# Optimization experiments

Measured on AMD Instinct MI355X. Metric: run time of the kernel, lower is better.

Reference implementation:

```python
import jax, jax.numpy as jnp
import numpy as np

B, C, U, N = 8, 64, 3, 512


def setup_inputs() -> dict:
    key = jax.random.key(0)
    k1, k2, k3, k4 = jax.random.split(key, 4)
    x = jax.random.normal(k1, (B, C, U, N), dtype=jnp.float32)
    # nn.Linear weights [out, in], applied as x @ W.T over channel dim
    s = 1.0 / np.sqrt(C)
    Wq = jax.random.uniform(k2, (C, C), dtype=jnp.float32, minval=-s, maxval=s)
    Wk = jax.random.uniform(k3, (C, C), dtype=jnp.float32, minval=-s, maxval=s)
    Wv = jax.random.uniform(k4, (C, C), dtype=jnp.float32, minval=-s, maxval=s)
    return {"x": x, "Wq": Wq, "Wk": Wk, "Wv": Wv}


def reference(x, Wq, Wk, Wv):
    # VNLinear: Linear over channel dim (dim 1), no bias: out[b,d,u,n] = sum_c x[b,c,u,n] W[d,c]
    def vn_linear(t, W):
        return jnp.einsum('bcun,dc->bdun', t, W)

    q = vn_linear(x, Wq)
    k = vn_linear(x, Wk)
    v = vn_linear(x, Wv)
    scale = x.shape[1] ** (-0.5)  # in_channels^-0.5
    # contraction over tiny vector-neuron dim u=3
    attn_logits = jnp.einsum('bcui,bcuj->bcij', q, k) * scale  # [B,C,N,N]
    attn_weights = jax.nn.softmax(attn_logits, axis=-1)
    out = jnp.einsum('bcij,bcuj->bcui', attn_weights, v)  # [B,C,U,N]
    return x + out
```

## Files before the change

### kernel.cpp

```cpp
#include <hip/hip_runtime.h>

#define BB 8
#define CC 64
#define UU 3
#define NN 512
#define POS (UU * NN)
#define QKV_ELEMS (BB * CC * POS)
#define SCALE2 0.1803368801111793f

__global__ __launch_bounds__(256) void proj_kernel(
    const float* __restrict__ x,
    const float* __restrict__ Wq,
    const float* __restrict__ Wk,
    const float* __restrict__ Wv,
    float* __restrict__ ws)
{
    const int blk   = blockIdx.x;
    const int bd2   = blk / 6;
    const int chunk = blk % 6;
    const int b     = bd2 >> 5;
    const int d0    = (bd2 & 31) * 2;
    const int tid   = threadIdx.x;
    const int p     = chunk * 256 + tid;

    __shared__ float w[6][CC];
    if (tid < 128) {
        int r = tid >> 6, c = tid & 63;
        w[r][c]     = Wq[(d0 + r) * CC + c];
        w[2 + r][c] = Wk[(d0 + r) * CC + c];
        w[4 + r][c] = Wv[(d0 + r) * CC + c];
    }
    __syncthreads();

    const float* xb = x + (size_t)b * CC * POS + p;
    float q0 = 0.f, q1 = 0.f, k0 = 0.f, k1 = 0.f, v0 = 0.f, v1 = 0.f;
    #pragma unroll 8
    for (int c = 0; c < CC; ++c) {
        float xv = xb[c * POS];
        q0 = fmaf(xv, w[0][c], q0);
        q1 = fmaf(xv, w[1][c], q1);
        k0 = fmaf(xv, w[2][c], k0);
        k1 = fmaf(xv, w[3][c], k1);
        v0 = fmaf(xv, w[4][c], v0);
        v1 = fmaf(xv, w[5][c], v1);
    }

    float* qs = ws;
    float* ks = ws + QKV_ELEMS;
    float* vs = ws + 2 * QKV_ELEMS;
    size_t base = (size_t)(b * CC + d0) * POS + p;
    qs[base] = q0 * SCALE2;  qs[base + POS] = q1 * SCALE2;
    ks[base] = k0;           ks[base + POS] = k1;
    vs[base] = v0;           vs[base + POS] = v1;
}

__global__ __launch_bounds__(256) void attn_kernel(
    const float* __restrict__ x,
    const float* __restrict__ ws,
    float* __restrict__ out)
{
    const int blk  = blockIdx.x;
    const int bd   = blk >> 1;
    const int half = blk & 1;
    const int tid  = threadIdx.x;

    __shared__ __align__(16) float ks[UU][NN];
    __shared__ __align__(16) float vs[UU][NN];
    __shared__ float4 part[NN / 2];

    const float* qsg = ws + (size_t)bd * POS;
    const float* ksg = ws + QKV_ELEMS     + (size_t)bd * POS;
    const float* vsg = ws + 2 * QKV_ELEMS + (size_t)bd * POS;

    {
        const float4* kg4 = (const float4*)ksg;
        const float4* vg4 = (const float4*)vsg;
        float4* ks4 = (float4*)&ks[0][0];
        float4* vs4 = (float4*)&vs[0][0];
        #pragma unroll
        for (int it = 0; it < 3; ++it) {
            int idx = tid + it * 256;
            if (idx < 384) ks4[idx] = kg4[idx];
            else           vs4[idx - 384] = vg4[idx - 384];
        }
    }
    __syncthreads();

    const int h    = tid & 3;
    const int slot = tid >> 2;

    float q0[4], q1[4], q2[4];
    #pragma unroll
    for (int m = 0; m < 4; ++m) {
        int i = half * 256 + slot + m * 64;
        q0[m] = qsg[i];
        q1[m] = qsg[NN + i];
        q2[m] = qsg[2 * NN + i];
    }

    float l[4]  = {0.f, 0.f, 0.f, 0.f};
    float a0[4] = {0.f, 0.f, 0.f, 0.f};
    float a1[4] = {0.f, 0.f, 0.f, 0.f};
    float a2[4] = {0.f, 0.f, 0.f, 0.f};

    const float4* k0p = (const float4*)&ks[0][0] + h * 32;
    const float4* k1p = (const float4*)&ks[1][0] + h * 32;
    const float4* k2p = (const float4*)&ks[2][0] + h * 32;
    const float4* v0p = (const float4*)&vs[0][0] + h * 32;
    const float4* v1p = (const float4*)&vs[1][0] + h * 32;
    const float4* v2p = (const float4*)&vs[2][0] + h * 32;
    const int t0 = 2 * h;

    #pragma unroll 2
    for (int tt = 0; tt < 32; ++tt) {
        const int t = (tt + t0) & 31;
        float4 k0 = k0p[t];
        float4 k1 = k1p[t];
        float4 k2 = k2p[t];
        float4 v0 = v0p[t];
        float4 v1 = v1p[t];
        float4 v2 = v2p[t];

        #pragma unroll
        for (int m = 0; m < 4; ++m) {
            float s0 = fmaf(q0[m], k0.x, fmaf(q1[m], k1.x, q2[m] * k2.x));
            float s1 = fmaf(q0[m], k0.y, fmaf(q1[m], k1.y, q2[m] * k2.y));
            float s2 = fmaf(q0[m], k0.z, fmaf(q1[m], k1.z, q2[m] * k2.z));
            float s3 = fmaf(q0[m], k0.w, fmaf(q1[m], k1.w, q2[m] * k2.w));

            float p0 = __builtin_amdgcn_exp2f(s0);
            float p1 = __builtin_amdgcn_exp2f(s1);
            float p2 = __builtin_amdgcn_exp2f(s2);
            float p3 = __builtin_amdgcn_exp2f(s3);

            l[m] += (p0 + p1) + (p2 + p3);
            a0[m] = fmaf(p0, v0.x, fmaf(p1, v0.y, fmaf(p2, v0.z, fmaf(p3, v0.w, a0[m]))));
            a1[m] = fmaf(p0, v1.x, fmaf(p1, v1.y, fmaf(p2, v1.z, fmaf(p3, v1.w, a1[m]))));
            a2[m] = fmaf(p0, v2.x, fmaf(p1, v2.y, fmaf(p2, v2.z, fmaf(p3, v2.w, a2[m]))));
        }
    }

    #pragma unroll
    for (int m = 0; m < 4; ++m) {
        l[m]  += __shfl_xor(l[m],  1);  l[m]  += __shfl_xor(l[m],  2);
        a0[m] += __shfl_xor(a0[m], 1);  a0[m] += __shfl_xor(a0[m], 2);
        a1[m] += __shfl_xor(a1[m], 1);  a1[m] += __shfl_xor(a1[m], 2);
        a2[m] += __shfl_xor(a2[m], 1);  a2[m] += __shfl_xor(a2[m], 2);
    }
    if (h == 0) {
        #pragma unroll
        for (int m = 0; m < 4; ++m) {
            part[slot + m * 64] = make_float4(a0[m], a1[m], a2[m], l[m]);
        }
    }
    __syncthreads();

    const int i = half * 256 + tid;
    float4 P = part[tid];
    float inv = 1.0f / P.w;
    const float* xd = x   + (size_t)bd * POS;
    float*       od = out + (size_t)bd * POS;
    od[i]          = xd[i]          + P.x * inv;
    od[NN + i]     = xd[NN + i]     + P.y * inv;
    od[2 * NN + i] = xd[2 * NN + i] + P.z * inv;
}

__global__ __launch_bounds__(256) void vn_attn_fused(
    const float* __restrict__ x,
    const float* __restrict__ Wq,
    const float* __restrict__ Wk,
    const float* __restrict__ Wv,
    float* __restrict__ out)
{
    const int bd  = blockIdx.x;
    const int b   = bd / CC;
    const int d   = bd % CC;
    const int tid = threadIdx.x;

    __shared__ float wq[CC], wk[CC], wv[CC];
    __shared__ float qs[UU][NN];
    __shared__ float ks[UU][NN];
    __shared__ float vs[UU][NN];

    if (tid < CC) {
        wq[tid] = Wq[d * CC + tid];
        wk[tid] = Wk[d * CC + tid];
        wv[tid] = Wv[d * CC + tid];
    }
    __syncthreads();

    const float* xb = x + (size_t)b * CC * POS;
    for (int p = tid; p < POS; p += 256) {
        float qa = 0.f, ka = 0.f, va = 0.f;
        #pragma unroll 8
        for (int c = 0; c < CC; ++c) {
            float xv = xb[c * POS + p];
            qa = fmaf(xv, wq[c], qa);
            ka = fmaf(xv, wk[c], ka);
            va = fmaf(xv, wv[c], va);
        }
        int u = p >> 9, n = p & (NN - 1);
        qs[u][n] = qa * SCALE2;
        ks[u][n] = ka;
        vs[u][n] = va;
    }
    __syncthreads();

    for (int i = tid; i < NN; i += 256) {
        float q0 = qs[0][i], q1 = qs[1][i], q2 = qs[2][i];
        float l = 0.f, a0 = 0.f, a1 = 0.f, a2 = 0.f;
        for (int j = 0; j < NN; j += 4) {
            float4 k0 = *(const float4*)&ks[0][j];
            float4 k1 = *(const float4*)&ks[1][j];
            float4 k2 = *(const float4*)&ks[2][j];
            float4 v0 = *(const float4*)&vs[0][j];
            float4 v1 = *(const float4*)&vs[1][j];
            float4 v2 = *(const float4*)&vs[2][j];
            float s0 = fmaf(q0, k0.x, fmaf(q1, k1.x, q2 * k2.x));
            float s1 = fmaf(q0, k0.y, fmaf(q1, k1.y, q2 * k2.y));
            float s2 = fmaf(q0, k0.z, fmaf(q1, k1.z, q2 * k2.z));
            float s3 = fmaf(q0, k0.w, fmaf(q1, k1.w, q2 * k2.w));
            float p0 = __builtin_amdgcn_exp2f(s0);
            float p1 = __builtin_amdgcn_exp2f(s1);
            float p2 = __builtin_amdgcn_exp2f(s2);
            float p3 = __builtin_amdgcn_exp2f(s3);
            l += p0 + p1 + p2 + p3;
            a0 = fmaf(p0, v0.x, fmaf(p1, v0.y, fmaf(p2, v0.z, fmaf(p3, v0.w, a0))));
            a1 = fmaf(p0, v1.x, fmaf(p1, v1.y, fmaf(p2, v1.z, fmaf(p3, v1.w, a1))));
            a2 = fmaf(p0, v2.x, fmaf(p1, v2.y, fmaf(p2, v2.z, fmaf(p3, v2.w, a2))));
        }
        float inv = 1.0f / l;
        size_t obase = ((size_t)(b * CC + d) * UU) * NN + i;
        const float* xd = xb + (size_t)d * POS;
        out[obase]          = xd[i]          + a0 * inv;
        out[obase + NN]     = xd[NN + i]     + a1 * inv;
        out[obase + 2 * NN] = xd[2 * NN + i] + a2 * inv;
    }
}

extern "C" void kernel_launch(void* const* d_in, const int* in_sizes, int n_in,
                              void* d_out, int out_size, void* d_ws, size_t ws_size,
                              hipStream_t stream) {
    const float* x  = (const float*)d_in[0];
    const float* Wq = (const float*)d_in[1];
    const float* Wk = (const float*)d_in[2];
    const float* Wv = (const float*)d_in[3];
    float* out = (float*)d_out;

    if (ws_size >= (size_t)3 * QKV_ELEMS * sizeof(float)) {
        float* ws = (float*)d_ws;
        proj_kernel<<<dim3(BB * 32 * 6), dim3(256), 0, stream>>>(x, Wq, Wk, Wv, ws);
        attn_kernel<<<dim3(BB * CC * 2), dim3(256), 0, stream>>>(x, ws, out);
    } else {
        vn_attn_fused<<<dim3(BB * CC), dim3(256), 0, stream>>>(x, Wq, Wk, Wv, out);
    }
}
```

Baseline: 105.3 us.

## Use packed float2 FMA in attention and widen projection to four outputs

The attention inner loop is rewritten with two-wide float vectors so the compiler can emit packed FP32 FMA/add instructions (v_pk_fma_f32), roughly halving the ALU instruction count for the score and accumulation math. The projection kernel now computes four output channels per thread, reads weights directly from global memory (uniform loads) instead of shared memory, and launches half as many blocks. The attention kernel also gets a launch-bounds occupancy hint. Costs are more register pressure and per-element extraction for exp2, plus changed summation order.

```diff
diff --git a/kernel.cpp b/kernel.cpp
--- a/kernel.cpp
+++ b/kernel.cpp
@@ -7,6 +7,8 @@
 #define POS (UU * NN)
 #define QKV_ELEMS (BB * CC * POS)
 #define SCALE2 0.1803368801111793f
+
+typedef float f2 __attribute__((ext_vector_type(2)));
 
 __global__ __launch_bounds__(256) void proj_kernel(
     const float* __restrict__ x,
@@ -16,45 +18,45 @@
     float* __restrict__ ws)
 {
     const int blk   = blockIdx.x;
-    const int bd2   = blk / 6;
+    const int bq    = blk / 6;
     const int chunk = blk % 6;
-    const int b     = bd2 >> 5;
-    const int d0    = (bd2 & 31) * 2;
-    const int tid   = threadIdx.x;
-    const int p     = chunk * 256 + tid;
-
-    __shared__ float w[6][CC];
-    if (tid < 128) {
-        int r = tid >> 6, c = tid & 63;
-        w[r][c]     = Wq[(d0 + r) * CC + c];
-        w[2 + r][c] = Wk[(d0 + r) * CC + c];
-        w[4 + r][c] = Wv[(d0 + r) * CC + c];
-    }
-    __syncthreads();
-
+    const int b     = bq >> 4;
+    const int d0    = (bq & 15) * 4;
+    const int p     = chunk * 256 + threadIdx.x;
+
+    const float* wq = Wq + (size_t)d0 * CC;
+    const float* wk = Wk + (size_t)d0 * CC;
+    const float* wv = Wv + (size_t)d0 * CC;
     const float* xb = x + (size_t)b * CC * POS + p;
-    float q0 = 0.f, q1 = 0.f, k0 = 0.f, k1 = 0.f, v0 = 0.f, v1 = 0.f;
-    #pragma unroll 8
+
+    float qa[4] = {0.f, 0.f, 0.f, 0.f};
+    float ka[4] = {0.f, 0.f, 0.f, 0.f};
+    float va[4] = {0.f, 0.f, 0.f, 0.f};
+
+    #pragma unroll 4
     for (int c = 0; c < CC; ++c) {
         float xv = xb[c * POS];
-        q0 = fmaf(xv, w[0][c], q0);
-        q1 = fmaf(xv, w[1][c], q1);
-        k0 = fmaf(xv, w[2][c], k0);
-        k1 = fmaf(xv, w[3][c], k1);
-        v0 = fmaf(xv, w[4][c], v0);
-        v1 = fmaf(xv, w[5][c], v1);
+        #pragma unroll
+        for (int r = 0; r < 4; ++r) {
+            qa[r] = fmaf(xv, wq[r * CC + c], qa[r]);
+            ka[r] = fmaf(xv, wk[r * CC + c], ka[r]);
+            va[r] = fmaf(xv, wv[r * CC + c], va[r]);
+        }
     }
 
     float* qs = ws;
     float* ks = ws + QKV_ELEMS;
     float* vs = ws + 2 * QKV_ELEMS;
-    size_t base = (size_t)(b * CC + d0) * POS + p;
-    qs[base] = q0 * SCALE2;  qs[base + POS] = q1 * SCALE2;
-    ks[base] = k0;           ks[base + POS] = k1;
-    vs[base] = v0;           vs[base + POS] = v1;
-}
-
-__global__ __launch_bounds__(256) void attn_kernel(
+    #pragma unroll
+    for (int r = 0; r < 4; ++r) {
+        size_t base = (size_t)(b * CC + d0 + r) * POS + p;
+        qs[base] = qa[r] * SCALE2;
+        ks[base] = ka[r];
+        vs[base] = va[r];
+    }
+}
+
+__global__ __launch_bounds__(256, 4) void attn_kernel(
     const float* __restrict__ x,
     const float* __restrict__ ws,
     float* __restrict__ out)
@@ -89,19 +91,22 @@
     const int h    = tid & 3;
     const int slot = tid >> 2;
 
-    float q0[4], q1[4], q2[4];
+    f2 Q0[4], Q1[4], Q2[4];
     #pragma unroll
     for (int m = 0; m < 4; ++m) {
         int i = half * 256 + slot + m * 64;
-        q0[m] = qsg[i];
-        q1[m] = qsg[NN + i];
-        q2[m] = qsg[2 * NN + i];
-    }
-
-    float l[4]  = {0.f, 0.f, 0.f, 0.f};
-    float a0[4] = {0.f, 0.f, 0.f, 0.f};
-    float a1[4] = {0.f, 0.f, 0.f, 0.f};
-    float a2[4] = {0.f, 0.f, 0.f, 0.f};
+        float a = qsg[i], b = qsg[NN + i], c = qsg[2 * NN + i];
+        Q0[m] = (f2){a, a};
+        Q1[m] = (f2){b, b};
+        Q2[m] = (f2){c, c};
+    }
+
+    f2 L[4], A0[4], A1[4], A2[4];
+    #pragma unroll
+    for (int m = 0; m < 4; ++m) {
+        L[m] = (f2){0.f, 0.f};  A0[m] = (f2){0.f, 0.f};
+        A1[m] = (f2){0.f, 0.f}; A2[m] = (f2){0.f, 0.f};
+    }
 
     const float4* k0p = (const float4*)&ks[0][0] + h * 32;
     const float4* k1p = (const float4*)&ks[1][0] + h * 32;
@@ -121,37 +126,46 @@
         float4 v1 = v1p[t];
         float4 v2 = v2p[t];
 
+        f2 k0a = (f2){k0.x, k0.y}, k0b = (f2){k0.z, k0.w};
+        f2 k1a = (f2){k1.x, k1.y}, k1b = (f2){k1.z, k1.w};
+        f2 k2a = (f2){k2.x, k2.y}, k2b = (f2){k2.z, k2.w};
+        f2 v0a = (f2){v0.x, v0.y}, v0b = (f2){v0.z, v0.w};
+        f2 v1a = (f2){v1.x, v1.y}, v1b = (f2){v1.z, v1.w};
+        f2 v2a = (f2){v2.x, v2.y}, v2b = (f2){v2.z, v2.w};
+
         #pragma unroll
         for (int m = 0; m < 4; ++m) {
-            float s0 = fmaf(q0[m], k0.x, fmaf(q1[m], k1.x, q2[m] * k2.x));
-            float s1 = fmaf(q0[m], k0.y, fmaf(q1[m], k1.y, q2[m] * k2.y));
-            float s2 = fmaf(q0[m], k0.z, fmaf(q1[m], k1.z, q2[m] * k2.z));
-            float s3 = fmaf(q0[m], k0.w, fmaf(q1[m], k1.w, q2[m] * k2.w));
-
-            float p0 = __builtin_amdgcn_exp2f(s0);
-            float p1 = __builtin_amdgcn_exp2f(s1);
-            float p2 = __builtin_amdgcn_exp2f(s2);
-            float p3 = __builtin_amdgcn_exp2f(s3);
-
-            l[m] += (p0 + p1) + (p2 + p3);
-            a0[m] = fmaf(p0, v0.x, fmaf(p1, v0.y, fmaf(p2, v0.z, fmaf(p3, v0.w, a0[m]))));
-            a1[m] = fmaf(p0, v1.x, fmaf(p1, v1.y, fmaf(p2, v1.z, fmaf(p3, v1.w, a1[m]))));
-            a2[m] = fmaf(p0, v2.x, fmaf(p1, v2.y, fmaf(p2, v2.z, fmaf(p3, v2.w, a2[m]))));
+            f2 sa = __builtin_elementwise_fma(Q0[m], k0a,
+                     __builtin_elementwise_fma(Q1[m], k1a, Q2[m] * k2a));
+            f2 sb = __builtin_elementwise_fma(Q0[m], k0b,
+                     __builtin_elementwise_fma(Q1[m], k1b, Q2[m] * k2b));
+
+            f2 pa = (f2){__builtin_amdgcn_exp2f(sa.x), __builtin_amdgcn_exp2f(sa.y)};
+            f2 pb = (f2){__builtin_amdgcn_exp2f(sb.x), __builtin_amdgcn_exp2f(sb.y)};
+
+            L[m]  = L[m] + pa + pb;
+            A0[m] = __builtin_elementwise_fma(pa, v0a,
+                      __builtin_elementwise_fma(pb, v0b, A0[m]));
+            A1[m] = __builtin_elementwise_fma(pa, v1a,
+                      __builtin_elementwise_fma(pb, v1b, A1[m]));
+            A2[m] = __builtin_elementwise_fma(pa, v2a,
+                      __builtin_elementwise_fma(pb, v2b, A2[m]));
         }
     }
 
     #pragma unroll
     for (int m = 0; m < 4; ++m) {
-        l[m]  += __shfl_xor(l[m],  1);  l[m]  += __shfl_xor(l[m],  2);
-        a0[m] += __shfl_xor(a0[m], 1);  a0[m] += __shfl_xor(a0[m], 2);
-        a1[m] += __shfl_xor(a1[m], 1);  a1[m] += __shfl_xor(a1[m], 2);
-        a2[m] += __shfl_xor(a2[m], 1);  a2[m] += __shfl_xor(a2[m], 2);
-    }
-    if (h == 0) {
-        #pragma unroll
-        for (int m = 0; m < 4; ++m) {
-            part[slot + m * 64] = make_float4(a0[m], a1[m], a2[m], l[m]);
-        }
+        float l  = L[m].x  + L[m].y;
+        float a0 = A0[m].x + A0[m].y;
+        float a1 = A1[m].x + A1[m].y;
+        float a2 = A2[m].x + A2[m].y;
+
+        l  += __shfl_xor(l,  1);  l  += __shfl_xor(l,  2);
+        a0 += __shfl_xor(a0, 1);  a0 += __shfl_xor(a0, 2);
+        a1 += __shfl_xor(a1, 1);  a1 += __shfl_xor(a1, 2);
+        a2 += __shfl_xor(a2, 1);  a2 += __shfl_xor(a2, 2);
+
+        if (h == 0) part[slot + m * 64] = make_float4(a0, a1, a2, l);
     }
     __syncthreads();
 
@@ -249,7 +263,7 @@
 
     if (ws_size >= (size_t)3 * QKV_ELEMS * sizeof(float)) {
         float* ws = (float*)d_ws;
-        proj_kernel<<<dim3(BB * 32 * 6), dim3(256), 0, stream>>>(x, Wq, Wk, Wv, ws);
+        proj_kernel<<<dim3(8 * 16 * 6), dim3(256), 0, stream>>>(x, Wq, Wk, Wv, ws);
         attn_kernel<<<dim3(BB * CC * 2), dim3(256), 0, stream>>>(x, ws, out);
     } else {
         vn_attn_fused<<<dim3(BB * CC), dim3(256), 0, stream>>>(x, Wq, Wk, Wv, out);
```

Result: faster. 98.39 us (-6.6%).
